# Kernel optimization log

Hardware: AMD Instinct MI355X
Metric: run time of the kernel (lower is better)

## Reference

```python
import jax, jax.numpy as jnp
import numpy as np

N = 100000      # nodes
E = 1600000     # edges
G = 256         # graphs in the batch
D_IN = 128
H = 128
C = 10
EPS = 1e-5      # BatchNorm eps


def setup_inputs() -> dict:
    key = jax.random.key(0)
    ks = jax.random.split(key, 32)
    inp = {
        'x': jax.random.normal(ks[0], (N, D_IN), jnp.float32),
        'edge_index': jax.random.randint(ks[1], (2, E), 0, N, dtype=jnp.int64),
        'batch': jnp.sort(jax.random.randint(ks[2], (N,), 0, G, dtype=jnp.int64)),
        'w1': jax.random.normal(ks[3], (D_IN, H), jnp.float32) * 0.05,
        'b1': jax.random.normal(ks[4], (H,), jnp.float32) * 0.05,
        'w2': jax.random.normal(ks[5], (H, H), jnp.float32) * 0.05,
        'b2': jax.random.normal(ks[6], (H,), jnp.float32) * 0.05,
        'w3': jax.random.normal(ks[7], (H, H), jnp.float32) * 0.05,
        'b3': jax.random.normal(ks[8], (H,), jnp.float32) * 0.05,
        'g1': jax.random.uniform(ks[9], (H,), jnp.float32, 0.5, 1.5),
        'be1': jax.random.normal(ks[10], (H,), jnp.float32) * 0.05,
        'm1': jax.random.normal(ks[11], (H,), jnp.float32) * 0.05,
        'v1': jax.random.uniform(ks[12], (H,), jnp.float32, 0.5, 1.5),
        'g2': jax.random.uniform(ks[13], (H,), jnp.float32, 0.5, 1.5),
        'be2': jax.random.normal(ks[14], (H,), jnp.float32) * 0.05,
        'm2': jax.random.normal(ks[15], (H,), jnp.float32) * 0.05,
        'v2': jax.random.uniform(ks[16], (H,), jnp.float32, 0.5, 1.5),
        'g3': jax.random.uniform(ks[17], (H,), jnp.float32, 0.5, 1.5),
        'be3': jax.random.normal(ks[18], (H,), jnp.float32) * 0.05,
        'm3': jax.random.normal(ks[19], (H,), jnp.float32) * 0.05,
        'v3': jax.random.uniform(ks[20], (H,), jnp.float32, 0.5, 1.5),
        'fcw1': jax.random.normal(ks[21], (H, H // 2), jnp.float32) * 0.05,
        'fcb1': jax.random.normal(ks[22], (H // 2,), jnp.float32) * 0.05,
        'fcw2': jax.random.normal(ks[23], (H // 2, C), jnp.float32) * 0.05,
        'fcb2': jax.random.normal(ks[24], (C,), jnp.float32) * 0.05,
    }
    return inp


def _gcn_norm(edge_index, n_nodes):
    # add self loops (PyG GCNConv default) and compute D^-1/2 (A+I) D^-1/2 norms
    loop = jnp.arange(n_nodes, dtype=edge_index.dtype)
    src = jnp.concatenate([edge_index[0], loop])
    dst = jnp.concatenate([edge_index[1], loop])
    deg = jax.ops.segment_sum(jnp.ones_like(dst, dtype=jnp.float32), dst, num_segments=n_nodes)
    dinv = jnp.where(deg > 0, jax.lax.rsqrt(deg), 0.0)
    norm = dinv[src] * dinv[dst]  # [E+N]
    return src, dst, norm


def _gcn_conv(x, W, b, src, dst, norm, n_nodes):
    h = x @ W                                   # [N, H]
    msg = norm[:, None] * h[src]                # gather + scale, [E+N, H]
    return jax.ops.segment_sum(msg, dst, num_segments=n_nodes) + b


def _bn_eval(x, gamma, beta, mean, var):
    return (x - mean) * jax.lax.rsqrt(var + EPS) * gamma + beta


def reference(x, edge_index, batch, w1, b1, w2, b2, w3, b3,
              g1, be1, m1, v1, g2, be2, m2, v2, g3, be3, m3, v3,
              fcw1, fcb1, fcw2, fcb2):
    n = x.shape[0]
    x = jnp.nan_to_num(x, nan=0.0, posinf=1e6, neginf=-1e6)
    src, dst, norm = _gcn_norm(edge_index, n)

    h = jax.nn.relu(_bn_eval(_gcn_conv(x, w1, b1, src, dst, norm, n), g1, be1, m1, v1))
    h = jax.nn.relu(_bn_eval(_gcn_conv(h, w2, b2, src, dst, norm, n), g2, be2, m2, v2))
    h = jax.nn.relu(_bn_eval(_gcn_conv(h, w3, b3, src, dst, norm, n), g3, be3, m3, v3))

    # global_mean_pool over graphs
    sums = jax.ops.segment_sum(h, batch, num_segments=G)            # [G, H]
    cnts = jax.ops.segment_sum(jnp.ones((n,), h.dtype), batch, num_segments=G)
    pooled = sums / jnp.maximum(cnts, 1.0)[:, None]

    out = jax.nn.relu(pooled @ fcw1 + fcb1) @ fcw2 + fcb2           # [G, C]
    return out
```

## Files before the change

### kernel.cpp

```cpp
#include <hip/hip_runtime.h>
#include <math.h>

#define NN 100000
#define EE 1600000
#define GG 256
#define HH 128
#define BSH 8
#define NBK 391
#define PASSA_WG 391
#define CAPB 6144

typedef __attribute__((ext_vector_type(8))) short short8;
typedef __attribute__((ext_vector_type(4))) float f32x4;

union U4S8 { uint4 u; short8 s; };

static __device__ __forceinline__ unsigned bf16rne(float f) {
    const unsigned u = __float_as_uint(f);
    return (u + 0x7fffu + ((u >> 16) & 1u)) >> 16;
}
static __device__ __forceinline__ unsigned packbf(float a, float b) {
    return bf16rne(a) | (bf16rne(b) << 16);
}
static __device__ __forceinline__ float bflo(unsigned u) { return __uint_as_float(u << 16); }
static __device__ __forceinline__ float bfhi(unsigned u) { return __uint_as_float(u & 0xffff0000u); }

__global__ __launch_bounds__(256) void setup_k(
    const int* __restrict__ ei, const int* __restrict__ batch,
    const float* __restrict__ w1, const float* __restrict__ w2,
    const float* __restrict__ w3,
    const float* __restrict__ b1, const float* __restrict__ g1,
    const float* __restrict__ be1, const float* __restrict__ m1,
    const float* __restrict__ v1,
    const float* __restrict__ b2, const float* __restrict__ g2,
    const float* __restrict__ be2, const float* __restrict__ m2,
    const float* __restrict__ v2,
    const float* __restrict__ b3, const float* __restrict__ g3,
    const float* __restrict__ be3, const float* __restrict__ m3,
    const float* __restrict__ v3,
    unsigned* __restrict__ bt, float* __restrict__ sc, float* __restrict__ sh,
    int* __restrict__ cursor, float* __restrict__ psum, int* __restrict__ gcnt,
    int* __restrict__ flags) {
    const int id = blockIdx.x * 256 + threadIdx.x;
    if (id < 24576) {
        const int w = id >> 13;
        const int rem = id & 8191;
        const int n = rem >> 6;
        const int kk = rem & 63;
        const float* W = (w == 0) ? w1 : (w == 1) ? w2 : w3;
        bt[id] = packbf(W[(2 * kk) * HH + n], W[(2 * kk + 1) * HH + n]);
    } else if (id < 24704) {
        const int c = id - 24576;
        float s;
        s = g1[c] / sqrtf(v1[c] + 1e-5f);
        sc[c] = s;           sh[c] = (b1[c] - m1[c]) * s + be1[c];
        s = g2[c] / sqrtf(v2[c] + 1e-5f);
        sc[128 + c] = s;     sh[128 + c] = (b2[c] - m2[c]) * s + be2[c];
        s = g3[c] / sqrtf(v3[c] + 1e-5f);
        sc[256 + c] = s;     sh[256 + c] = (b3[c] - m3[c]) * s + be3[c];
    } else if (id < 25095) {
        const int b = id - 24704;
        cursor[b] = b * CAPB;
    } else if (id < 57863) {
        psum[id - 25095] = 0.0f;
    } else if (id < 58119) {
        gcnt[id - 57863] = 0;
    } else if (id == 58119) {
        int e64 = 1;
        for (int j = 0; j < 8; ++j) {
            if (ei[2 * EE - 1 - 2 * j] != 0) { e64 = 0; break; }
        }
        flags[0] = e64;
        flags[1] = (batch[NN - 1] == 0) ? 1 : 0;
    }
}
#define SETUP_GRID 228

__global__ __launch_bounds__(256) void passA_k(const int* __restrict__ ei,
                                               const int* __restrict__ flags,
                                               int* __restrict__ cursor,
                                               unsigned* __restrict__ pairs) {
    __shared__ int h[NBK];
    __shared__ int rbase[NBK];
    const int tid = threadIdx.x;
    for (int i = tid; i < NBK; i += 256) h[i] = 0;
    __syncthreads();
    const bool e64 = flags[0] != 0;
    const int base = blockIdx.x * 4096;
    int scache[16], dcache[16];
#pragma unroll
    for (int j = 0; j < 16; ++j) {
        const int e = base + j * 256 + tid;
        int s = -1, d = 0;
        if (e < EE) {
            s = e64 ? ei[2 * e] : ei[e];
            d = e64 ? ei[2 * (EE + e)] : ei[EE + e];
            atomicAdd(&h[d >> BSH], 1);
        }
        scache[j] = s; dcache[j] = d;
    }
    __syncthreads();
    for (int i = tid; i < NBK; i += 256) {
        const int c = h[i];
        rbase[i] = c ? atomicAdd(&cursor[i], c) : 0;
    }
    __syncthreads();
    for (int i = tid; i < NBK; i += 256) h[i] = 0;
    __syncthreads();
#pragma unroll
    for (int j = 0; j < 16; ++j) {
        const int s = scache[j];
        if (s >= 0) {
            const int d = dcache[j];
            const int b = d >> BSH;
            const int r = atomicAdd(&h[b], 1);
            pairs[rbase[b] + r] = ((unsigned)(d & 255) << 17) | (unsigned)s;
        }
    }
}

__global__ __launch_bounds__(256) void passB_k(const unsigned* __restrict__ pairs,
                                               const int* __restrict__ cursor,
                                               int* __restrict__ offs,
                                               int* __restrict__ degcnt,
                                               float* __restrict__ dinv,
                                               int* __restrict__ csr) {
    __shared__ unsigned pk[CAPB];
    __shared__ int cnt[256];
    __shared__ int loff[256];
    __shared__ int sc[256];
    const int tid = threadIdx.x;
    const int b = blockIdx.x;
    const int p0 = b * CAPB;
    const int np = cursor[b] - p0;
    const int nb0 = b << BSH;
    const int nnode = (NN - nb0 < 256) ? (NN - nb0) : 256;

    cnt[tid] = 0;
    __syncthreads();
    for (int i = tid; i < np; i += 256) {
        const unsigned p = pairs[p0 + i];
        pk[i] = p;
        atomicAdd(&cnt[p >> 17], 1);
    }
    __syncthreads();
    const int creal = cnt[tid];
    const int cpad = (tid < nnode) ? ((creal + 8) & ~7) : 0;
    sc[tid] = cpad;
    __syncthreads();
    for (int off = 1; off < 256; off <<= 1) {
        int t = (tid >= off) ? sc[tid - off] : 0;
        __syncthreads();
        sc[tid] += t;
        __syncthreads();
    }
    const int ex = sc[tid] - cpad;
    loff[tid] = ex;
    if (tid < nnode) {
        const int node = nb0 + tid;
        offs[node] = p0 + ex;
        degcnt[node] = creal;
        dinv[node] = 1.0f / sqrtf((float)(creal + 1));
    }
    __syncthreads();
    cnt[tid] = 0;
    __syncthreads();
    for (int i = tid; i < np; i += 256) {
        const unsigned p = pk[i];
        const int dl = (int)(p >> 17);
        const int r = atomicAdd(&cnt[dl], 1);
        csr[p0 + loff[dl] + r] = (int)(p & 0x1FFFFu);
    }
    if (tid < nnode) {
        const int basep = p0 + loff[tid];
        csr[basep + creal] = nb0 + tid;
        for (int j = creal + 1; j < cpad; ++j) csr[basep + j] = NN;
    }
}

static __device__ __forceinline__ float sani(float v) {
    if (isnan(v)) return 0.0f;
    if (isinf(v)) return v > 0.0f ? 1e6f : -1e6f;
    return v;
}

template <bool AF32>
__global__ __launch_bounds__(256) void gemm_mfma_k(const float* __restrict__ Af,
                                                   const unsigned* __restrict__ Abf,
                                                   const unsigned* __restrict__ btg,
                                                   const float* __restrict__ dinv,
                                                   unsigned* __restrict__ C, int M) {
    __shared__ unsigned lds_u[8704];
    const int tid = threadIdx.x;
    const int wave = tid >> 6;
    const int lane = tid & 63;
    const int nl = lane & 15;
    const int q = lane >> 4;
    const int row0 = blockIdx.x * 64 + wave * 16;
    const int rowg = row0 + nl;
    const int rowa = min(rowg, M - 1);

    {
        const uint4* __restrict__ bg4 = (const uint4*)btg;
        for (int i = tid; i < 2048; i += 256) {
            const int n = i >> 4, w4 = i & 15;
            *(uint4*)&lds_u[n * 68 + w4 * 4] = bg4[n * 16 + w4];
        }
    }

    short8 a[4];
    if (AF32) {
#pragma unroll
        for (int ks = 0; ks < 4; ++ks) {
            const float4 p = *(const float4*)(Af + (size_t)rowa * HH + ks * 32 + q * 8);
            const float4 r = *(const float4*)(Af + (size_t)rowa * HH + ks * 32 + q * 8 + 4);
            U4S8 cv;
            cv.u = make_uint4(packbf(sani(p.x), sani(p.y)), packbf(sani(p.z), sani(p.w)),
                              packbf(sani(r.x), sani(r.y)), packbf(sani(r.z), sani(r.w)));
            a[ks] = cv.s;
        }
    } else {
#pragma unroll
        for (int ks = 0; ks < 4; ++ks) {
            U4S8 cv;
            cv.u = *(const uint4*)(Abf + (size_t)rowa * 64 + ks * 16 + q * 4);
            a[ks] = cv.s;
        }
    }

    __syncthreads();

    f32x4 acc[8];
#pragma unroll
    for (int t = 0; t < 8; ++t) acc[t] = (f32x4)0.0f;

    const unsigned short* __restrict__ bts = (const unsigned short*)lds_u;
#pragma unroll
    for (int ks = 0; ks < 4; ++ks) {
#pragma unroll
        for (int t = 0; t < 8; ++t) {
            const int n = t * 16 + nl;
            const short8 b = *(const short8*)(bts + n * 136 + ks * 32 + q * 8);
            acc[t] = __builtin_amdgcn_mfma_f32_16x16x32_bf16(b, a[ks], acc[t], 0, 0, 0);
        }
    }

    if (rowg < M) {
        const float dsc = dinv[rowg];
        unsigned* crow = C + (size_t)rowg * 64;
#pragma unroll
        for (int t = 0; t < 8; ++t) {
            uint2 o;
            o.x = packbf(dsc * acc[t][0], dsc * acc[t][1]);
            o.y = packbf(dsc * acc[t][2], dsc * acc[t][3]);
            *(uint2*)(crow + t * 8 + q * 2) = o;
        }
    } else if (rowg == M) {
        unsigned* crow = C + (size_t)M * 64;
#pragma unroll
        for (int t = 0; t < 8; ++t)
            *(uint2*)(crow + t * 8 + q * 2) = make_uint2(0u, 0u);
    }
}

__global__ __launch_bounds__(256) void aggregate_k(
    const unsigned* __restrict__ hpre, const int* __restrict__ csr,
    const int* __restrict__ offs, const int* __restrict__ cnt,
    const float* __restrict__ dinv,
    const float* __restrict__ bnsc, const float* __restrict__ bnsh,
    unsigned* __restrict__ xout) {
    const int v = __builtin_amdgcn_readfirstlane(blockIdx.x * 4 + (threadIdx.x >> 6));
    const int lane = threadIdx.x & 63;
    const int cg = lane & 15;
    const int sub = lane >> 4;
    const int c8 = cg * 8;

    const float dv = dinv[v];
    const int start = offs[v];
    const int npad = (cnt[v] + 8) & ~7;
    const char* __restrict__ hb = (const char*)hpre;
    const unsigned cgo = (unsigned)(cg << 4);

    float acc[8];
#pragma unroll
    for (int j = 0; j < 8; ++j) acc[j] = 0.0f;

    int i = 0;
    for (; i + 16 <= npad; i += 16) {
        const int sA = csr[start + i + sub];
        const int sB = csr[start + i + 4 + sub];
        const int sC = csr[start + i + 8 + sub];
        const int sD = csr[start + i + 12 + sub];
        const uint4 rA = *(const uint4*)(hb + (((unsigned)sA << 8) | cgo));
        const uint4 rB = *(const uint4*)(hb + (((unsigned)sB << 8) | cgo));
        const uint4 rC = *(const uint4*)(hb + (((unsigned)sC << 8) | cgo));
        const uint4 rD = *(const uint4*)(hb + (((unsigned)sD << 8) | cgo));
        acc[0] += (bflo(rA.x) + bflo(rB.x)) + (bflo(rC.x) + bflo(rD.x));
        acc[1] += (bfhi(rA.x) + bfhi(rB.x)) + (bfhi(rC.x) + bfhi(rD.x));
        acc[2] += (bflo(rA.y) + bflo(rB.y)) + (bflo(rC.y) + bflo(rD.y));
        acc[3] += (bfhi(rA.y) + bfhi(rB.y)) + (bfhi(rC.y) + bfhi(rD.y));
        acc[4] += (bflo(rA.z) + bflo(rB.z)) + (bflo(rC.z) + bflo(rD.z));
        acc[5] += (bfhi(rA.z) + bfhi(rB.z)) + (bfhi(rC.z) + bfhi(rD.z));
        acc[6] += (bflo(rA.w) + bflo(rB.w)) + (bflo(rC.w) + bflo(rD.w));
        acc[7] += (bfhi(rA.w) + bfhi(rB.w)) + (bfhi(rC.w) + bfhi(rD.w));
    }
    if (i < npad) {
        const int sA = csr[start + i + sub];
        const int sB = csr[start + i + 4 + sub];
        const uint4 rA = *(const uint4*)(hb + (((unsigned)sA << 8) | cgo));
        const uint4 rB = *(const uint4*)(hb + (((unsigned)sB << 8) | cgo));
        acc[0] += bflo(rA.x) + bflo(rB.x);
        acc[1] += bfhi(rA.x) + bfhi(rB.x);
        acc[2] += bflo(rA.y) + bflo(rB.y);
        acc[3] += bfhi(rA.y) + bfhi(rB.y);
        acc[4] += bflo(rA.z) + bflo(rB.z);
        acc[5] += bfhi(rA.z) + bfhi(rB.z);
        acc[6] += bflo(rA.w) + bflo(rB.w);
        acc[7] += bfhi(rA.w) + bfhi(rB.w);
    }

#pragma unroll
    for (int j = 0; j < 8; ++j) {
        acc[j] += __shfl_xor(acc[j], 16);
        acc[j] += __shfl_xor(acc[j], 32);
    }

    if (sub == 0) {
        const float4 sca = *(const float4*)(bnsc + c8);
        const float4 scb = *(const float4*)(bnsc + c8 + 4);
        const float4 sha = *(const float4*)(bnsh + c8);
        const float4 shb = *(const float4*)(bnsh + c8 + 4);
        const float y0 = fmaxf(dv * acc[0] * sca.x + sha.x, 0.0f);
        const float y1 = fmaxf(dv * acc[1] * sca.y + sha.y, 0.0f);
        const float y2 = fmaxf(dv * acc[2] * sca.z + sha.z, 0.0f);
        const float y3 = fmaxf(dv * acc[3] * sca.w + sha.w, 0.0f);
        const float y4 = fmaxf(dv * acc[4] * scb.x + shb.x, 0.0f);
        const float y5 = fmaxf(dv * acc[5] * scb.y + shb.y, 0.0f);
        const float y6 = fmaxf(dv * acc[6] * scb.z + shb.z, 0.0f);
        const float y7 = fmaxf(dv * acc[7] * scb.w + shb.w, 0.0f);
        *(uint4*)(xout + (size_t)v * 64 + cg * 4) =
            make_uint4(packbf(y0, y1), packbf(y2, y3), packbf(y4, y5), packbf(y6, y7));
    }
}

__global__ __launch_bounds__(256) void pool_sum_k(
    const unsigned* __restrict__ x, const int* __restrict__ batch,
    const int* __restrict__ flags, float* __restrict__ psum,
    int* __restrict__ gcnt) {
    const int wave = threadIdx.x >> 6;
    const int lane = threadIdx.x & 63;
    const int row0 = blockIdx.x * 64 + wave * 16;
    if (row0 >= NN) return;
    const bool b64 = flags[1] != 0;

    float sx = 0.0f, sy = 0.0f;
    int cur = -1, runlen = 0;
#pragma unroll
    for (int r = 0; r < 16; ++r) {
        const int row = row0 + r;
        if (row >= NN) break;
        const int g = b64 ? batch[2 * row] : batch[row];
        if (g != cur) {
            if (cur >= 0) {
                atomicAdd(&psum[cur * HH + lane * 2 + 0], sx);
                atomicAdd(&psum[cur * HH + lane * 2 + 1], sy);
                if (lane == 0) atomicAdd(&gcnt[cur], runlen);
            }
            cur = g; sx = 0.0f; sy = 0.0f; runlen = 0;
        }
        const unsigned u = x[(size_t)row * 64 + lane];
        sx += bflo(u);
        sy += bfhi(u);
        ++runlen;
    }
    if (cur >= 0) {
        atomicAdd(&psum[cur * HH + lane * 2 + 0], sx);
        atomicAdd(&psum[cur * HH + lane * 2 + 1], sy);
        if (lane == 0) atomicAdd(&gcnt[cur], runlen);
    }
}

__global__ __launch_bounds__(128) void head_k(
    const float* __restrict__ psum, const int* __restrict__ gcnt,
    const float* __restrict__ fw1, const float* __restrict__ fb1,
    const float* __restrict__ fw2, const float* __restrict__ fb2,
    float* __restrict__ out) {
    __shared__ float pooled[128];
    __shared__ float hid[64];
    const int g = blockIdx.x;
    const int tid = threadIdx.x;

    const int cntn = gcnt[g];
    pooled[tid] = psum[g * HH + tid] / (float)(cntn > 0 ? cntn : 1);
    __syncthreads();

    if (tid < 64) {
        float a = fb1[tid];
#pragma unroll 4
        for (int k = 0; k < 128; ++k) a += pooled[k] * fw1[k * 64 + tid];
        hid[tid] = fmaxf(a, 0.0f);
    }
    __syncthreads();
    if (tid < 10) {
        float a = fb2[tid];
#pragma unroll
        for (int k = 0; k < 64; ++k) a += hid[k] * fw2[k * 10 + tid];
        out[g * 10 + tid] = a;
    }
}

extern "C" void kernel_launch(void* const* d_in, const int* in_sizes, int n_in,
                              void* d_out, int out_size, void* d_ws, size_t ws_size,
                              hipStream_t stream) {
    const float* x_in  = (const float*)d_in[0];
    const int*   ei    = (const int*)d_in[1];
    const int*   batch = (const int*)d_in[2];
    const float* w1 = (const float*)d_in[3];
    const float* b1 = (const float*)d_in[4];
    const float* w2 = (const float*)d_in[5];
    const float* b2 = (const float*)d_in[6];
    const float* w3 = (const float*)d_in[7];
    const float* b3 = (const float*)d_in[8];
    const float* g1 = (const float*)d_in[9];
    const float* be1 = (const float*)d_in[10];
    const float* m1 = (const float*)d_in[11];
    const float* v1 = (const float*)d_in[12];
    const float* g2 = (const float*)d_in[13];
    const float* be2 = (const float*)d_in[14];
    const float* m2 = (const float*)d_in[15];
    const float* v2 = (const float*)d_in[16];
    const float* g3 = (const float*)d_in[17];
    const float* be3 = (const float*)d_in[18];
    const float* m3 = (const float*)d_in[19];
    const float* v3 = (const float*)d_in[20];
    const float* fw1 = (const float*)d_in[21];
    const float* fb1 = (const float*)d_in[22];
    const float* fw2 = (const float*)d_in[23];
    const float* fb2 = (const float*)d_in[24];
    float* out = (float*)d_out;

    size_t off = 0;
    char* base = (char*)d_ws;
    auto alloc = [&](size_t bytes) -> void* {
        void* p = base + off;
        off += (bytes + 255) & ~(size_t)255;
        return p;
    };
    int*      degcnt = (int*)alloc((size_t)NN * 4);
    float*    dinv   = (float*)alloc((size_t)NN * 4);
    int*      offs   = (int*)alloc((size_t)NN * 4);
    int*      cursor = (int*)alloc((size_t)NBK * 4);
    int*      flags  = (int*)alloc(256);
    float*    bnsc   = (float*)alloc(3 * 128 * 4);
    float*    bnsh   = (float*)alloc(3 * 128 * 4);
    unsigned* btg    = (unsigned*)alloc(3 * 8192 * 4);
    float*    psum   = (float*)alloc((size_t)GG * HH * 4);
    int*      gcnt   = (int*)alloc((size_t)GG * 4);
    int*      csr    = (int*)alloc((size_t)NBK * CAPB * 4);
    unsigned* pairs  = (unsigned*)alloc((size_t)NBK * CAPB * 4);
    unsigned* bufx   = (unsigned*)alloc((size_t)NN * 64 * 4);
    unsigned* hpre   = (unsigned*)alloc((size_t)(NN + 1) * 64 * 4);
    if (off > ws_size) return;

    setup_k<<<SETUP_GRID, 256, 0, stream>>>(ei, batch, w1, w2, w3,
                                            b1, g1, be1, m1, v1,
                                            b2, g2, be2, m2, v2,
                                            b3, g3, be3, m3, v3,
                                            btg, bnsc, bnsh, cursor, psum, gcnt,
                                            flags);
    passA_k<<<PASSA_WG, 256, 0, stream>>>(ei, flags, cursor, pairs);
    passB_k<<<NBK, 256, 0, stream>>>(pairs, cursor, offs, degcnt, dinv, csr);

    const int ggrid = (NN + 63) / 64;
    const int agrid = NN / 4;

    gemm_mfma_k<true><<<ggrid, 256, 0, stream>>>(x_in, nullptr, btg, dinv, hpre, NN);
    aggregate_k<<<agrid, 256, 0, stream>>>(hpre, csr, offs, degcnt, dinv,
                                           bnsc, bnsh, bufx);
    gemm_mfma_k<false><<<ggrid, 256, 0, stream>>>(nullptr, bufx, btg + 8192, dinv, hpre, NN);
    aggregate_k<<<agrid, 256, 0, stream>>>(hpre, csr, offs, degcnt, dinv,
                                           bnsc + 128, bnsh + 128, bufx);
    gemm_mfma_k<false><<<ggrid, 256, 0, stream>>>(nullptr, bufx, btg + 16384, dinv, hpre, NN);
    aggregate_k<<<agrid, 256, 0, stream>>>(hpre, csr, offs, degcnt, dinv,
                                           bnsc + 256, bnsh + 256, bufx);

    pool_sum_k<<<ggrid, 256, 0, stream>>>(bufx, batch, flags, psum, gcnt);
    head_k<<<GG, 128, 0, stream>>>(psum, gcnt, fw1, fb1, fw2, fb2, out);
}
```

Measured before the change: 440.3 us.

## Fuse aggregation with next layer's GEMM into a single kernel

Adds agg_gemm_k, which aggregates 16 nodes per block, applies BN+ReLU, stages the bf16 rows in LDS, and multiplies by the next layer's weights with MFMA before writing scaled hpre. This replaces the aggregate→bufx→gemm round trip for layers 2 and 3, removing two launches and one write plus one read of the intermediate node-feature matrix per fused layer. The cost is that each block reads B weights straight from global memory without LDS reuse. Blocks also do serial per-wave gathers over 4 nodes, which may lower the gather parallelism per block.

```diff
diff --git a/kernel.cpp b/kernel.cpp
--- a/kernel.cpp
+++ b/kernel.cpp
@@ -184,9 +184,7 @@
     return v;
 }
 
-template <bool AF32>
 __global__ __launch_bounds__(256) void gemm_mfma_k(const float* __restrict__ Af,
-                                                   const unsigned* __restrict__ Abf,
                                                    const unsigned* __restrict__ btg,
                                                    const float* __restrict__ dinv,
                                                    unsigned* __restrict__ C, int M) {
@@ -209,23 +207,14 @@
     }
 
     short8 a[4];
-    if (AF32) {
-#pragma unroll
-        for (int ks = 0; ks < 4; ++ks) {
-            const float4 p = *(const float4*)(Af + (size_t)rowa * HH + ks * 32 + q * 8);
-            const float4 r = *(const float4*)(Af + (size_t)rowa * HH + ks * 32 + q * 8 + 4);
-            U4S8 cv;
-            cv.u = make_uint4(packbf(sani(p.x), sani(p.y)), packbf(sani(p.z), sani(p.w)),
-                              packbf(sani(r.x), sani(r.y)), packbf(sani(r.z), sani(r.w)));
-            a[ks] = cv.s;
-        }
-    } else {
-#pragma unroll
-        for (int ks = 0; ks < 4; ++ks) {
-            U4S8 cv;
-            cv.u = *(const uint4*)(Abf + (size_t)rowa * 64 + ks * 16 + q * 4);
-            a[ks] = cv.s;
-        }
+#pragma unroll
+    for (int ks = 0; ks < 4; ++ks) {
+        const float4 p = *(const float4*)(Af + (size_t)rowa * HH + ks * 32 + q * 8);
+        const float4 r = *(const float4*)(Af + (size_t)rowa * HH + ks * 32 + q * 8 + 4);
+        U4S8 cv;
+        cv.u = make_uint4(packbf(sani(p.x), sani(p.y)), packbf(sani(p.z), sani(p.w)),
+                          packbf(sani(r.x), sani(r.y)), packbf(sani(r.z), sani(r.w)));
+        a[ks] = cv.s;
     }
 
     __syncthreads();
@@ -261,6 +250,127 @@
         for (int t = 0; t < 8; ++t)
             *(uint2*)(crow + t * 8 + q * 2) = make_uint2(0u, 0u);
     }
+}
+
+__global__ __launch_bounds__(256) void agg_gemm_k(
+    const unsigned* __restrict__ hin, const int* __restrict__ csr,
+    const int* __restrict__ offs, const int* __restrict__ cnt,
+    const float* __restrict__ dinv,
+    const float* __restrict__ bnsc, const float* __restrict__ bnsh,
+    const unsigned* __restrict__ btg,
+    unsigned* __restrict__ hout) {
+    __shared__ unsigned ybuf[16 * 68];
+    const int tid = threadIdx.x;
+    const int wave = tid >> 6;
+    const int lane = tid & 63;
+    const int cg = lane & 15;
+    const int sub = lane >> 4;
+    const int c8 = cg * 8;
+    const char* __restrict__ hb = (const char*)hin;
+    const unsigned cgo = (unsigned)(cg << 4);
+
+    if (blockIdx.x == 0 && tid < 64) hout[(size_t)NN * 64 + tid] = 0u;
+
+    const float4 sca = *(const float4*)(bnsc + c8);
+    const float4 scb = *(const float4*)(bnsc + c8 + 4);
+    const float4 sha = *(const float4*)(bnsh + c8);
+    const float4 shb = *(const float4*)(bnsh + c8 + 4);
+
+    for (int i = 0; i < 4; ++i) {
+        const int v = __builtin_amdgcn_readfirstlane(blockIdx.x * 16 + wave * 4 + i);
+        const float dv = dinv[v];
+        const int start = offs[v];
+        const int npad = (cnt[v] + 8) & ~7;
+
+        float acc[8];
+#pragma unroll
+        for (int j = 0; j < 8; ++j) acc[j] = 0.0f;
+
+        int e = 0;
+        for (; e + 16 <= npad; e += 16) {
+            const int sA = csr[start + e + sub];
+            const int sB = csr[start + e + 4 + sub];
+            const int sC = csr[start + e + 8 + sub];
+            const int sD = csr[start + e + 12 + sub];
+            const uint4 rA = *(const uint4*)(hb + (((unsigned)sA << 8) | cgo));
+            const uint4 rB = *(const uint4*)(hb + (((unsigned)sB << 8) | cgo));
+            const uint4 rC = *(const uint4*)(hb + (((unsigned)sC << 8) | cgo));
+            const uint4 rD = *(const uint4*)(hb + (((unsigned)sD << 8) | cgo));
+            acc[0] += (bflo(rA.x) + bflo(rB.x)) + (bflo(rC.x) + bflo(rD.x));
+            acc[1] += (bfhi(rA.x) + bfhi(rB.x)) + (bfhi(rC.x) + bfhi(rD.x));
+            acc[2] += (bflo(rA.y) + bflo(rB.y)) + (bflo(rC.y) + bflo(rD.y));
+            acc[3] += (bfhi(rA.y) + bfhi(rB.y)) + (bfhi(rC.y) + bfhi(rD.y));
+            acc[4] += (bflo(rA.z) + bflo(rB.z)) + (bflo(rC.z) + bflo(rD.z));
+            acc[5] += (bfhi(rA.z) + bfhi(rB.z)) + (bfhi(rC.z) + bfhi(rD.z));
+            acc[6] += (bflo(rA.w) + bflo(rB.w)) + (bflo(rC.w) + bflo(rD.w));
+            acc[7] += (bfhi(rA.w) + bfhi(rB.w)) + (bfhi(rC.w) + bfhi(rD.w));
+        }
+        if (e < npad) {
+            const int sA = csr[start + e + sub];
+            const int sB = csr[start + e + 4 + sub];
+            const uint4 rA = *(const uint4*)(hb + (((unsigned)sA << 8) | cgo));
+            const uint4 rB = *(const uint4*)(hb + (((unsigned)sB << 8) | cgo));
+            acc[0] += bflo(rA.x) + bflo(rB.x);
+            acc[1] += bfhi(rA.x) + bfhi(rB.x);
+            acc[2] += bflo(rA.y) + bflo(rB.y);
+            acc[3] += bfhi(rA.y) + bfhi(rB.y);
+            acc[4] += bflo(rA.z) + bflo(rB.z);
+            acc[5] += bfhi(rA.z) + bfhi(rB.z);
+            acc[6] += bflo(rA.w) + bflo(rB.w);
+            acc[7] += bfhi(rA.w) + bfhi(rB.w);
+        }
+
+#pragma unroll
+        for (int j = 0; j < 8; ++j) {
+            acc[j] += __shfl_xor(acc[j], 16);
+            acc[j] += __shfl_xor(acc[j], 32);
+        }
+
+        if (sub == 0) {
+            const float y0 = fmaxf(dv * acc[0] * sca.x + sha.x, 0.0f);
+            const float y1 = fmaxf(dv * acc[1] * sca.y + sha.y, 0.0f);
+            const float y2 = fmaxf(dv * acc[2] * sca.z + sha.z, 0.0f);
+            const float y3 = fmaxf(dv * acc[3] * sca.w + sha.w, 0.0f);
+            const float y4 = fmaxf(dv * acc[4] * scb.x + shb.x, 0.0f);
+            const float y5 = fmaxf(dv * acc[5] * scb.y + shb.y, 0.0f);
+            const float y6 = fmaxf(dv * acc[6] * scb.z + shb.z, 0.0f);
+            const float y7 = fmaxf(dv * acc[7] * scb.w + shb.w, 0.0f);
+            *(uint4*)&ybuf[(wave * 4 + i) * 68 + cg * 4] =
+                make_uint4(packbf(y0, y1), packbf(y2, y3), packbf(y4, y5), packbf(y6, y7));
+        }
+    }
+    __syncthreads();
+
+    const int nl = cg;
+    const int q = sub;
+    short8 arow[4];
+#pragma unroll
+    for (int ks = 0; ks < 4; ++ks) {
+        U4S8 cv;
+        cv.u = *(const uint4*)&ybuf[nl * 68 + ks * 16 + q * 4];
+        arow[ks] = cv.s;
+    }
+    const uint4* __restrict__ bt4 = (const uint4*)btg;
+    const int t0 = wave * 2;
+    f32x4 acc0 = (f32x4)0.0f, acc1 = (f32x4)0.0f;
+#pragma unroll
+    for (int ks = 0; ks < 4; ++ks) {
+        U4S8 b0, b1;
+        b0.u = bt4[((t0 + 0) * 16 + nl) * 16 + ks * 4 + q];
+        b1.u = bt4[((t0 + 1) * 16 + nl) * 16 + ks * 4 + q];
+        acc0 = __builtin_amdgcn_mfma_f32_16x16x32_bf16(b0.s, arow[ks], acc0, 0, 0, 0);
+        acc1 = __builtin_amdgcn_mfma_f32_16x16x32_bf16(b1.s, arow[ks], acc1, 0, 0, 0);
+    }
+    const int rowg = blockIdx.x * 16 + nl;
+    const float dsc = dinv[rowg];
+    unsigned* crow = hout + (size_t)rowg * 64;
+    uint2 o0, o1;
+    o0.x = packbf(dsc * acc0[0], dsc * acc0[1]);
+    o0.y = packbf(dsc * acc0[2], dsc * acc0[3]);
+    o1.x = packbf(dsc * acc1[0], dsc * acc1[1]);
+    o1.y = packbf(dsc * acc1[2], dsc * acc1[3]);
+    *(uint2*)(crow + (t0 + 0) * 8 + q * 2) = o0;
+    *(uint2*)(crow + (t0 + 1) * 8 + q * 2) = o1;
 }
 
 __global__ __launch_bounds__(256) void aggregate_k(
@@ -458,8 +568,8 @@
     int*      gcnt   = (int*)alloc((size_t)GG * 4);
     int*      csr    = (int*)alloc((size_t)NBK * CAPB * 4);
     unsigned* pairs  = (unsigned*)alloc((size_t)NBK * CAPB * 4);
-    unsigned* bufx   = (unsigned*)alloc((size_t)NN * 64 * 4);
-    unsigned* hpre   = (unsigned*)alloc((size_t)(NN + 1) * 64 * 4);
+    unsigned* bufA   = (unsigned*)alloc((size_t)(NN + 1) * 64 * 4);
+    unsigned* bufB   = (unsigned*)alloc((size_t)(NN + 1) * 64 * 4);
     if (off > ws_size) return;
 
     setup_k<<<SETUP_GRID, 256, 0, stream>>>(ei, batch, w1, w2, w3,
@@ -472,18 +582,17 @@
     passB_k<<<NBK, 256, 0, stream>>>(pairs, cursor, offs, degcnt, dinv, csr);
 
     const int ggrid = (NN + 63) / 64;
+    const int fgrid = NN / 16;
     const int agrid = NN / 4;
 
-    gemm_mfma_k<true><<<ggrid, 256, 0, stream>>>(x_in, nullptr, btg, dinv, hpre, NN);
-    aggregate_k<<<agrid, 256, 0, stream>>>(hpre, csr, offs, degcnt, dinv,
-                                           bnsc, bnsh, bufx);
-    gemm_mfma_k<false><<<ggrid, 256, 0, stream>>>(nullptr, bufx, btg + 8192, dinv, hpre, NN);
-    aggregate_k<<<agrid, 256, 0, stream>>>(hpre, csr, offs, degcnt, dinv,
-                                           bnsc + 128, bnsh + 128, bufx);
-    gemm_mfma_k<false><<<ggrid, 256, 0, stream>>>(nullptr, bufx, btg + 16384, dinv, hpre, NN);
-    aggregate_k<<<agrid, 256, 0, stream>>>(hpre, csr, offs, degcnt, dinv,
-                                           bnsc + 256, bnsh + 256, bufx);
-
-    pool_sum_k<<<ggrid, 256, 0, stream>>>(bufx, batch, flags, psum, gcnt);
+    gemm_mfma_k<<<ggrid, 256, 0, stream>>>(x_in, btg, dinv, bufA, NN);
+    agg_gemm_k<<<fgrid, 256, 0, stream>>>(bufA, csr, offs, degcnt, dinv,
+                                          bnsc, bnsh, btg + 8192, bufB);
+    agg_gemm_k<<<fgrid, 256, 0, stream>>>(bufB, csr, offs, degcnt, dinv,
+                                          bnsc + 128, bnsh + 128, btg + 16384, bufA);
+    aggregate_k<<<agrid, 256, 0, stream>>>(bufA, csr, offs, degcnt, dinv,
+                                           bnsc + 256, bnsh + 256, bufB);
+
+    pool_sum_k<<<ggrid, 256, 0, stream>>>(bufB, batch, flags, psum, gcnt);
     head_k<<<GG, 128, 0, stream>>>(psum, gcnt, fw1, fb1, fw2, fb2, out);
 }
```

Result: no change. 435.9 us (-1.0%).
